# Kernel optimization log

Hardware: AMD Instinct MI355X
Metric: run time of the kernel (lower is better)

The kernel has to match this reference:

```python
import jax, jax.numpy as jnp
import numpy as np

NEG_INF = -1e30


def _rotate_half(t):
    d = t.shape[-1] // 2
    t1, t2 = t[..., :d], t[..., d:]
    return jnp.concatenate([-t2, t1], axis=-1)


def _apply_rope(t, cos, sin):
    # t: [B, H, T, D]; cos/sin: [T, D] broadcast over B, H
    return t * cos[None, None, :, :] + _rotate_half(t) * sin[None, None, :, :]


def setup_inputs() -> dict:
    key = jax.random.key(0)
    ks = jax.random.split(key, 5)
    B, T, C, H = 2, 2048, 2048, 16
    D = C // H
    x = jax.random.normal(ks[0], (B, T, C), dtype=jnp.float32)
    # RoPE tables (realistic: derived from inv freqs)
    inv_freq = 1.0 / (10000.0 ** (jnp.arange(0, D, 2, dtype=jnp.float32) / D))
    freqs = jnp.arange(T, dtype=jnp.float32)[:, None] * inv_freq[None, :]
    emb = jnp.concatenate([freqs, freqs], axis=-1)  # [T, D]
    cos, sin = jnp.cos(emb), jnp.sin(emb)
    W_attn = jax.random.normal(ks[1], (C, 3 * C), dtype=jnp.float32) * (1.0 / np.sqrt(C))
    W_proj = jax.random.normal(ks[2], (C, C), dtype=jnp.float32) * (1.0 / np.sqrt(C))
    return {"x": x, "cos": cos, "sin": sin, "W_attn": W_attn, "W_proj": W_proj}


def reference(x, cos, sin, W_attn, W_proj):
    B, T, C = x.shape
    H = 16
    D = C // H
    qkv = x @ W_attn  # [B, T, 3C]
    q, k, v = jnp.split(qkv, 3, axis=-1)
    # [B, T, C] -> [B, H, T, D]
    to_heads = lambda t: t.reshape(B, T, H, D).transpose(0, 2, 1, 3)
    q, k, v = to_heads(q), to_heads(k), to_heads(v)
    q = _apply_rope(q, cos, sin)
    k = _apply_rope(k, cos, sin)
    scale = 1.0 / np.sqrt(D).astype(np.float32)
    scores = jnp.einsum("bhqd,bhkd->bhqk", q, k) * scale
    causal = jnp.tril(jnp.ones((T, T), dtype=bool))
    scores = jnp.where(causal[None, None, :, :], scores, NEG_INF)
    attn = jax.nn.softmax(scores, axis=-1)
    out = jnp.einsum("bhqk,bhkd->bhqd", attn, v)  # [B, H, T, D]
    out = out.transpose(0, 2, 1, 3).reshape(B, T, C)
    return out @ W_proj
```

## Files before the change

### kernel.cpp

```cpp
#include <hip/hip_runtime.h>
#include <stdint.h>

#define Bc   2
#define Tc   2048
#define Cc   2048
#define Hc   16
#define Dc   128
#define BT   4096
#define N3   6144
#define QSCALE 0.08838834764831845f

typedef _Float16 f16x8 __attribute__((ext_vector_type(8)));
typedef _Float16 f16x4 __attribute__((ext_vector_type(4)));
typedef float    f32x4 __attribute__((ext_vector_type(4)));

__device__ __forceinline__ void gload_lds16(const void* g, void* l) {
  __builtin_amdgcn_global_load_lds(
      (__attribute__((address_space(1))) void*)(uintptr_t)g,
      (__attribute__((address_space(3))) void*)(unsigned int)(uintptr_t)l,
      16, 0, 0);
}

__global__ __launch_bounds__(256) void cvt_f16_kernel(const float* __restrict__ in,
                                                      _Float16* __restrict__ out, int n4) {
  int i = blockIdx.x * 256 + threadIdx.x;
  if (i < n4) {
    float4 v = ((const float4*)in)[i];
    f16x4 o; o[0]=(_Float16)v.x; o[1]=(_Float16)v.y; o[2]=(_Float16)v.z; o[3]=(_Float16)v.w;
    ((f16x4*)out)[i] = o;
  }
}

__global__ __launch_bounds__(256) void transpose_cvt_kernel(const float* __restrict__ W,
                                                            _Float16* __restrict__ Wt,
                                                            int K, int N) {
  const int n0 = blockIdx.x * 64, k0 = blockIdx.y * 64;
  __shared__ float tile[64][65];
  const int tid = threadIdx.x;
  #pragma unroll
  for (int i = 0; i < 4; ++i) {
    int u = i * 256 + tid, r = u >> 4, s = u & 15;
    float4 v = *(const float4*)&W[(size_t)(k0 + r) * N + n0 + s * 4];
    tile[r][s*4+0] = v.x; tile[r][s*4+1] = v.y; tile[r][s*4+2] = v.z; tile[r][s*4+3] = v.w;
  }
  __syncthreads();
  #pragma unroll
  for (int i = 0; i < 2; ++i) {
    int u = i * 256 + tid, c = u >> 3, rg = u & 7;
    f16x8 o;
    #pragma unroll
    for (int j = 0; j < 8; ++j) o[j] = (_Float16)tile[rg * 8 + j][c];
    *(f16x8*)&Wt[(size_t)(n0 + c) * K + k0 + rg * 8] = o;
  }
}

#define GLDS_BUF 49152

template<bool OUT16>
__global__ __launch_bounds__(512, 2) void gemm256_kernel(const _Float16* __restrict__ A,
                                                         const _Float16* __restrict__ Bt,
                                                         void* __restrict__ C,
                                                         int M, int N, int K) {
  __shared__ __align__(16) char glds[2 * GLDS_BUF];
  const int tid = threadIdx.x;
  const int wid = tid >> 6, lane = tid & 63, g = lane >> 4, c16 = lane & 15;
  const int wr = wid >> 1, wc = wid & 1;

  const int nblocks = gridDim.x, chunk = nblocks >> 3;
  const int bid = blockIdx.x;
  const int sw = (bid & 7) * chunk + (bid >> 3);
  const int ntm = M >> 8;
  const int m0 = (sw % ntm) * 256, n0 = (sw / ntm) * 128;

  const int ntk = K >> 6;
  const int row8 = tid >> 3, s8 = tid & 7;
  const int scol = (s8 ^ (row8 & 7)) * 8;
  const int swz = (c16 & 7) << 4;

  auto stage_tile = [&](char* bb, int kt) {
    #pragma unroll
    for (int c = 0; c < 4; ++c)
      gload_lds16(A + (size_t)(m0 + c * 64 + row8) * K + kt * 64 + scol,
                  bb + c * 8192 + tid * 16);
    #pragma unroll
    for (int c = 0; c < 2; ++c)
      gload_lds16(Bt + (size_t)(n0 + c * 64 + row8) * K + kt * 64 + scol,
                  bb + 32768 + c * 8192 + tid * 16);
  };

  f32x4 acc[4][4] = {};

  stage_tile(glds, 0);
  stage_tile(glds + GLDS_BUF, 1);
  asm volatile("s_waitcnt vmcnt(6)" ::: "memory");
  __builtin_amdgcn_s_barrier();

  for (int t = 0; t < ntk; ++t) {
    char* bb = glds + (t & 1) * GLDS_BUF;

    f16x8 a0[4], b0[4];
    #pragma unroll
    for (int mi = 0; mi < 4; ++mi)
      a0[mi] = *(const f16x8*)(bb + (wr * 64 + mi * 16 + c16) * 128 + ((g * 16) ^ swz));
    #pragma unroll
    for (int ni = 0; ni < 4; ++ni)
      b0[ni] = *(const f16x8*)(bb + 32768 + (wc * 64 + ni * 16 + c16) * 128 + ((g * 16) ^ swz));
    __builtin_amdgcn_s_setprio(1);
    #pragma unroll
    for (int mi = 0; mi < 4; ++mi)
      #pragma unroll
      for (int ni = 0; ni < 4; ++ni)
        acc[mi][ni] = __builtin_amdgcn_mfma_f32_16x16x32_f16(a0[mi], b0[ni], acc[mi][ni], 0, 0, 0);
    __builtin_amdgcn_s_setprio(0);

    f16x8 a1[4], b1[4];
    #pragma unroll
    for (int mi = 0; mi < 4; ++mi)
      a1[mi] = *(const f16x8*)(bb + (wr * 64 + mi * 16 + c16) * 128 + ((64 + g * 16) ^ swz));
    #pragma unroll
    for (int ni = 0; ni < 4; ++ni)
      b1[ni] = *(const f16x8*)(bb + 32768 + (wc * 64 + ni * 16 + c16) * 128 + ((64 + g * 16) ^ swz));
    asm volatile("s_waitcnt lgkmcnt(0)" ::: "memory");
    __builtin_amdgcn_sched_barrier(0);
    __builtin_amdgcn_s_barrier();
    if (t + 2 < ntk) {
      stage_tile(bb, t + 2);
      asm volatile("s_waitcnt vmcnt(6)" ::: "memory");
    } else if (t + 1 < ntk) {
      asm volatile("s_waitcnt vmcnt(0)" ::: "memory");
    }
    __builtin_amdgcn_s_barrier();
    __builtin_amdgcn_s_setprio(1);
    #pragma unroll
    for (int mi = 0; mi < 4; ++mi)
      #pragma unroll
      for (int ni = 0; ni < 4; ++ni)
        acc[mi][ni] = __builtin_amdgcn_mfma_f32_16x16x32_f16(a1[mi], b1[ni], acc[mi][ni], 0, 0, 0);
    __builtin_amdgcn_s_setprio(0);
  }

  #pragma unroll
  for (int mi = 0; mi < 4; ++mi)
    #pragma unroll
    for (int ni = 0; ni < 4; ++ni) {
      int row = m0 + wr * 64 + mi * 16 + g * 4;
      int col = n0 + wc * 64 + ni * 16 + c16;
      #pragma unroll
      for (int r = 0; r < 4; ++r) {
        if constexpr (OUT16) ((_Float16*)C)[(size_t)(row + r) * N + col] = (_Float16)acc[mi][ni][r];
        else                 ((float*)C)[(size_t)(row + r) * N + col]    = acc[mi][ni][r];
      }
    }
}

__global__ __launch_bounds__(256) void rope_qk_kernel(const _Float16* __restrict__ qkv,
                                                      const float* __restrict__ cosT,
                                                      const float* __restrict__ sinT,
                                                      _Float16* __restrict__ Qr,
                                                      _Float16* __restrict__ Kr) {
  const int bt = blockIdx.x;
  const int b = bt >> 11, t = bt & 2047;
  const int tid = threadIdx.x;
  const _Float16* row = qkv + (size_t)bt * N3;
  const int sw = (t & 7) * 8;
  #pragma unroll
  for (int i = 0; i < 4; ++i) {
    int p = i * 256 + tid;
    int h = p >> 6, d = p & 63;
    float cs = cosT[t * Dc + d], sn = sinT[t * Dc + d];
    float ql = (float)row[h * Dc + d],        qh = (float)row[h * Dc + d + 64];
    float kl = (float)row[Cc + h * Dc + d],   kh = (float)row[Cc + h * Dc + d + 64];
    float q0 = ql * cs - qh * sn, q1 = qh * cs + ql * sn;
    float k0 = kl * cs - kh * sn, k1 = kh * cs + kl * sn;
    size_t obase = ((size_t)(b * Hc + h) * Tc + t) * Dc;
    Qr[obase + d]        = (_Float16)(q0 * QSCALE);
    Qr[obase + d + 64]   = (_Float16)(q1 * QSCALE);
    Kr[obase + (d ^ sw)]        = (_Float16)k0;
    Kr[obase + ((d + 64) ^ sw)] = (_Float16)k1;
  }
}

__global__ __launch_bounds__(256) void vtrans_kernel(const _Float16* __restrict__ qkv,
                                                     _Float16* __restrict__ Vt) {
  const int t0 = blockIdx.x * 64, d0 = blockIdx.y * 64, bh = blockIdx.z;
  const int b = bh >> 4, h = bh & 15;
  __shared__ __align__(16) _Float16 tile[64][72];
  const int tid = threadIdx.x;
  #pragma unroll
  for (int i = 0; i < 2; ++i) {
    int u = i * 256 + tid, tr = u >> 3, sg = u & 7;
    f16x8 v = *(const f16x8*)&qkv[((size_t)b * Tc + t0 + tr) * N3 + 2 * Cc + h * Dc + d0 + sg * 8];
    *(f16x8*)&tile[tr][sg * 8] = v;
  }
  __syncthreads();
  #pragma unroll
  for (int i = 0; i < 2; ++i) {
    int u = i * 256 + tid, dl = u >> 3, tg = u & 7;
    int d = d0 + dl;
    f16x8 o;
    #pragma unroll
    for (int j = 0; j < 8; ++j) o[j] = tile[tg * 8 + j][dl];
    size_t off = ((size_t)bh * Dc + d) * Tc + t0 + ((tg ^ (d & 7)) * 8);
    *(f16x8*)&Vt[off] = o;
  }
}

__global__ __launch_bounds__(256, 2) void attn_kernel(const _Float16* __restrict__ Qr,
                                                      const _Float16* __restrict__ Kr,
                                                      const _Float16* __restrict__ Vt,
                                                      _Float16* __restrict__ Oh) {
  const int bh = blockIdx.x;
  const int pr = blockIdx.y;
  const int qtA = pr, qtB = 31 - pr;
  const int tid = threadIdx.x;
  const int w = tid >> 6, lane = tid & 63, g = lane >> 4, c16 = lane & 15, l7 = lane & 7;
  const int rA = qtA * 64 + w * 16;
  const int rB = qtB * 64 + w * 16;

  __shared__ __align__(16) _Float16 Klds[2][64 * 128];
  __shared__ __align__(16) _Float16 Vlds[2][128 * 64];
  __shared__ __align__(16) _Float16 Plds[4][16][72];

  const _Float16* Qb = Qr + (size_t)bh * Tc * Dc;
  f16x8 qfA[4], qfB[4];
  #pragma unroll
  for (int kb = 0; kb < 4; ++kb) {
    qfA[kb] = *(const f16x8*)&Qb[(size_t)(rA + c16) * Dc + kb * 32 + g * 8];
    qfB[kb] = *(const f16x8*)&Qb[(size_t)(rB + c16) * Dc + kb * 32 + g * 8];
  }

  f32x4 accA[8] = {}, accB[8] = {};
  float mA[4], lA[4], mB[4], lB[4];
  #pragma unroll
  for (int r = 0; r < 4; ++r) { mA[r] = -1e30f; lA[r] = 0.f; mB[r] = -1e30f; lB[r] = 0.f; }

  const _Float16* Kt0 = Kr + (size_t)bh * Tc * Dc;

  auto stage = [&](int j, int buf) {
    const char* src = (const char*)(Kt0 + (size_t)j * 64 * Dc);
    #pragma unroll
    for (int i = 0; i < 4; ++i) {
      int ch = i * 4 + w;
      gload_lds16(src + ch * 1024 + lane * 16, (char*)(&Klds[buf][0]) + ch * 1024);
    }
    #pragma unroll
    for (int i = 0; i < 4; ++i) {
      int ch = i * 4 + w;
      int d = ch * 8 + (lane >> 3);
      const char* gs = (const char*)(Vt + ((size_t)bh * Dc + d) * Tc + j * 64) + (lane & 7) * 16;
      gload_lds16(gs, (char*)(&Vlds[buf][0]) + ch * 1024);
    }
  };

  auto process_tile = [&](f32x4* s, f32x4* acc, float* m, float* l,
                          int rT, int j, int cur, bool maskit) {
    if (maskit) {
      #pragma unroll
      for (int ni = 0; ni < 4; ++ni)
        #pragma unroll
        for (int r = 0; r < 4; ++r) {
          int q = rT + g * 4 + r;
          int kv = j * 64 + ni * 16 + c16;
          if (kv > q) s[ni][r] = -1e30f;
        }
    }
    #pragma unroll
    for (int r = 0; r < 4; ++r) {
      float mt = fmaxf(fmaxf(s[0][r], s[1][r]), fmaxf(s[2][r], s[3][r]));
      #pragma unroll
      for (int off = 1; off < 16; off <<= 1) mt = fmaxf(mt, __shfl_xor(mt, off));
      float mnew = fmaxf(m[r], mt);
      float alpha = __expf(m[r] - mnew);
      float p0 = __expf(s[0][r] - mnew), p1 = __expf(s[1][r] - mnew);
      float p2 = __expf(s[2][r] - mnew), p3 = __expf(s[3][r] - mnew);
      float ls = p0 + p1 + p2 + p3;
      #pragma unroll
      for (int off = 1; off < 16; off <<= 1) ls += __shfl_xor(ls, off);
      l[r] = l[r] * alpha + ls;
      m[r] = mnew;
      #pragma unroll
      for (int di = 0; di < 8; ++di) acc[di][r] *= alpha;
      int prow = g * 4 + r;
      Plds[w][prow][0  + c16] = (_Float16)p0;
      Plds[w][prow][16 + c16] = (_Float16)p1;
      Plds[w][prow][32 + c16] = (_Float16)p2;
      Plds[w][prow][48 + c16] = (_Float16)p3;
    }
    #pragma unroll
    for (int kvb = 0; kvb < 2; ++kvb) {
      f16x8 pf = *(const f16x8*)&Plds[w][c16][kvb * 32 + g * 8];
      __builtin_amdgcn_s_setprio(1);
      #pragma unroll
      for (int di = 0; di < 8; ++di) {
        f16x8 vf = *(const f16x8*)&Vlds[cur][(di * 16 + c16) * 64 + ((kvb * 4 + g) ^ l7) * 8];
        acc[di] = __builtin_amdgcn_mfma_f32_16x16x32_f16(pf, vf, acc[di], 0, 0, 0);
      }
      __builtin_amdgcn_s_setprio(0);
    }
  };

  const int nt = qtB + 1;
  stage(0, 0);
  __syncthreads();
  int cur = 0;
  for (int j = 0; j < nt; ++j) {
    if (j + 1 < nt) stage(j + 1, cur ^ 1);
    const bool doA = (j <= qtA);

    f32x4 sA[4] = {}, sB[4] = {};
    #pragma unroll
    for (int kb = 0; kb < 4; ++kb) {
      f16x8 bfr[4];
      #pragma unroll
      for (int ni = 0; ni < 4; ++ni)
        bfr[ni] = *(const f16x8*)&Klds[cur][(ni * 16 + c16) * 128 + ((kb * 4 + g) ^ l7) * 8];
      __builtin_amdgcn_s_setprio(1);
      #pragma unroll
      for (int ni = 0; ni < 4; ++ni) {
        sB[ni] = __builtin_amdgcn_mfma_f32_16x16x32_f16(qfB[kb], bfr[ni], sB[ni], 0, 0, 0);
        if (doA)
          sA[ni] = __builtin_amdgcn_mfma_f32_16x16x32_f16(qfA[kb], bfr[ni], sA[ni], 0, 0, 0);
      }
      __builtin_amdgcn_s_setprio(0);
    }

    process_tile(sB, accB, mB, lB, rB, j, cur, j == qtB);
    if (doA) process_tile(sA, accA, mA, lA, rA, j, cur, j == qtA);

    __syncthreads();
    cur ^= 1;
  }

  const int b = bh >> 4, h = bh & 15;
  #pragma unroll
  for (int tile = 0; tile < 2; ++tile) {
    f32x4* acc = tile ? accB : accA;
    float* l   = tile ? lB   : lA;
    int rT     = tile ? rB   : rA;
    #pragma unroll
    for (int r = 0; r < 4; ++r) {
      float inv = 1.0f / l[r];
      int trow = rT + g * 4 + r;
      _Float16* orow = Oh + ((size_t)b * Tc + trow) * Cc + h * Dc;
      #pragma unroll
      for (int di = 0; di < 8; ++di)
        orow[di * 16 + c16] = (_Float16)(acc[di][r] * inv);
    }
  }
}

extern "C" void kernel_launch(void* const* d_in, const int* in_sizes, int n_in,
                              void* d_out, int out_size, void* d_ws, size_t ws_size,
                              hipStream_t stream) {
  const float* x      = (const float*)d_in[0];
  const float* cosT   = (const float*)d_in[1];
  const float* sinT   = (const float*)d_in[2];
  const float* W_attn = (const float*)d_in[3];
  const float* W_proj = (const float*)d_in[4];
  float* out = (float*)d_out;

  const size_t OFF_XH   = 0;
  const size_t OFF_WAH  = 16777216;
  const size_t OFF_WPH  = 41943040;
  const size_t OFF_QKV  = 50331648;
  const size_t OFF_QR   = 100663296;
  const size_t OFF_KR   = 117440512;
  const size_t OFF_VT   = 134217728;
  const size_t WS_NEEDED = 150994944;
  if (ws_size < WS_NEEDED) return;

  char* ws = (char*)d_ws;
  _Float16* xh   = (_Float16*)(ws + OFF_XH);
  _Float16* Wah  = (_Float16*)(ws + OFF_WAH);
  _Float16* Wph  = (_Float16*)(ws + OFF_WPH);
  _Float16* qkvh = (_Float16*)(ws + OFF_QKV);
  _Float16* Qr   = (_Float16*)(ws + OFF_QR);
  _Float16* Kr   = (_Float16*)(ws + OFF_KR);
  _Float16* Vt   = (_Float16*)(ws + OFF_VT);
  _Float16* Oh   = qkvh;

  cvt_f16_kernel<<<dim3(8192), dim3(256), 0, stream>>>(x, xh, (Bc * Tc * Cc) / 4);
  transpose_cvt_kernel<<<dim3(N3 / 64, Cc / 64), dim3(256), 0, stream>>>(W_attn, Wah, Cc, N3);
  transpose_cvt_kernel<<<dim3(Cc / 64, Cc / 64), dim3(256), 0, stream>>>(W_proj, Wph, Cc, Cc);
  gemm256_kernel<true><<<dim3((BT / 256) * (N3 / 128)), dim3(512), 0, stream>>>(xh, Wah, qkvh, BT, N3, Cc);
  rope_qk_kernel<<<dim3(BT), dim3(256), 0, stream>>>(qkvh, cosT, sinT, Qr, Kr);
  vtrans_kernel<<<dim3(Tc / 64, Dc / 64, Bc * Hc), dim3(256), 0, stream>>>(qkvh, Vt);
  attn_kernel<<<dim3(Bc * Hc, 16), dim3(256), 0, stream>>>(Qr, Kr, Vt, Oh);
  gemm256_kernel<false><<<dim3((BT / 256) * (Cc / 128)), dim3(512), 0, stream>>>(Oh, Wph, out, BT, Cc, Cc);
}
```

Measured before the change: 405.9 us.

## Triple-buffer GEMM LDS tiles to overlap loads with second-half MFMAs

Switches the 256x128 GEMM from double to triple LDS buffering with rotating pointers. The next-next tile is issued into a free buffer right after the first half-K MFMAs, and the second-half fragment reads and MFMAs follow without a second barrier. The intent is to cut one barrier per iteration and hide global-to-LDS latency better. LDS use grows to 144KB, so launch bounds drop to one block per CU, losing the previous two-block occupancy.

```diff
diff --git a/kernel.cpp b/kernel.cpp
--- a/kernel.cpp
+++ b/kernel.cpp
@@ -57,11 +57,11 @@
 #define GLDS_BUF 49152
 
 template<bool OUT16>
-__global__ __launch_bounds__(512, 2) void gemm256_kernel(const _Float16* __restrict__ A,
+__global__ __launch_bounds__(512, 1) void gemm256_kernel(const _Float16* __restrict__ A,
                                                          const _Float16* __restrict__ Bt,
                                                          void* __restrict__ C,
                                                          int M, int N, int K) {
-  __shared__ __align__(16) char glds[2 * GLDS_BUF];
+  __shared__ __align__(16) char glds[3 * GLDS_BUF];
   const int tid = threadIdx.x;
   const int wid = tid >> 6, lane = tid & 63, g = lane >> 4, c16 = lane & 15;
   const int wr = wid >> 1, wc = wid & 1;
@@ -90,21 +90,24 @@
 
   f32x4 acc[4][4] = {};
 
-  stage_tile(glds, 0);
-  stage_tile(glds + GLDS_BUF, 1);
-  asm volatile("s_waitcnt vmcnt(6)" ::: "memory");
-  __builtin_amdgcn_s_barrier();
+  char* p0 = glds;
+  char* p1 = glds + GLDS_BUF;
+  char* p2 = glds + 2 * GLDS_BUF;
+  stage_tile(p0, 0);
+  stage_tile(p1, 1);
 
   for (int t = 0; t < ntk; ++t) {
-    char* bb = glds + (t & 1) * GLDS_BUF;
+    if (t < ntk - 1) asm volatile("s_waitcnt vmcnt(6)" ::: "memory");
+    else             asm volatile("s_waitcnt vmcnt(0)" ::: "memory");
+    __builtin_amdgcn_s_barrier();
 
     f16x8 a0[4], b0[4];
     #pragma unroll
     for (int mi = 0; mi < 4; ++mi)
-      a0[mi] = *(const f16x8*)(bb + (wr * 64 + mi * 16 + c16) * 128 + ((g * 16) ^ swz));
+      a0[mi] = *(const f16x8*)(p0 + (wr * 64 + mi * 16 + c16) * 128 + ((g * 16) ^ swz));
     #pragma unroll
     for (int ni = 0; ni < 4; ++ni)
-      b0[ni] = *(const f16x8*)(bb + 32768 + (wc * 64 + ni * 16 + c16) * 128 + ((g * 16) ^ swz));
+      b0[ni] = *(const f16x8*)(p0 + 32768 + (wc * 64 + ni * 16 + c16) * 128 + ((g * 16) ^ swz));
     __builtin_amdgcn_s_setprio(1);
     #pragma unroll
     for (int mi = 0; mi < 4; ++mi)
@@ -112,24 +115,19 @@
       for (int ni = 0; ni < 4; ++ni)
         acc[mi][ni] = __builtin_amdgcn_mfma_f32_16x16x32_f16(a0[mi], b0[ni], acc[mi][ni], 0, 0, 0);
     __builtin_amdgcn_s_setprio(0);
-
-    f16x8 a1[4], b1[4];
-    #pragma unroll
-    for (int mi = 0; mi < 4; ++mi)
-      a1[mi] = *(const f16x8*)(bb + (wr * 64 + mi * 16 + c16) * 128 + ((64 + g * 16) ^ swz));
-    #pragma unroll
-    for (int ni = 0; ni < 4; ++ni)
-      b1[ni] = *(const f16x8*)(bb + 32768 + (wc * 64 + ni * 16 + c16) * 128 + ((64 + g * 16) ^ swz));
     asm volatile("s_waitcnt lgkmcnt(0)" ::: "memory");
     __builtin_amdgcn_sched_barrier(0);
     __builtin_amdgcn_s_barrier();
-    if (t + 2 < ntk) {
-      stage_tile(bb, t + 2);
-      asm volatile("s_waitcnt vmcnt(6)" ::: "memory");
-    } else if (t + 1 < ntk) {
-      asm volatile("s_waitcnt vmcnt(0)" ::: "memory");
-    }
-    __builtin_amdgcn_s_barrier();
+
+    if (t + 2 < ntk) stage_tile(p2, t + 2);
+
+    f16x8 a1[4], b1[4];
+    #pragma unroll
+    for (int mi = 0; mi < 4; ++mi)
+      a1[mi] = *(const f16x8*)(p0 + (wr * 64 + mi * 16 + c16) * 128 + ((64 + g * 16) ^ swz));
+    #pragma unroll
+    for (int ni = 0; ni < 4; ++ni)
+      b1[ni] = *(const f16x8*)(p0 + 32768 + (wc * 64 + ni * 16 + c16) * 128 + ((64 + g * 16) ^ swz));
     __builtin_amdgcn_s_setprio(1);
     #pragma unroll
     for (int mi = 0; mi < 4; ++mi)
@@ -137,6 +135,10 @@
       for (int ni = 0; ni < 4; ++ni)
         acc[mi][ni] = __builtin_amdgcn_mfma_f32_16x16x32_f16(a1[mi], b1[ni], acc[mi][ni], 0, 0, 0);
     __builtin_amdgcn_s_setprio(0);
+    asm volatile("s_waitcnt lgkmcnt(0)" ::: "memory");
+    __builtin_amdgcn_sched_barrier(0);
+
+    char* tp = p0; p0 = p1; p1 = p2; p2 = tp;
   }
 
   #pragma unroll
```

Measured after the change: 421.9 us. +3.9%, slower.
